# Kernel tuning notes

Hardware: AMD Instinct MI355X
Metric: run time of the kernel (lower is better)

Reference implementation:

```python
import jax, jax.numpy as jnp
import numpy as np

N_KW, N_RT = 100000, 20000
D, H, O = 128, 128, 128
E_A, E_B, E_C = 1600000, 1600000, 320000


def setup_inputs() -> dict:
    key = jax.random.key(0)
    ks = jax.random.split(key, 32)
    inp = {
        "x_kw": jax.random.normal(ks[0], (N_KW, D), jnp.float32),
        "x_rt": jax.random.normal(ks[1], (N_RT, D), jnp.float32),
        "src_a": jax.random.randint(ks[2], (E_A,), 0, N_RT),
        "dst_a": jax.random.randint(ks[3], (E_A,), 0, N_KW),
        "src_b": jax.random.randint(ks[4], (E_B,), 0, N_KW),
        "dst_b": jax.random.randint(ks[5], (E_B,), 0, N_KW),
        "src_c": jax.random.randint(ks[6], (E_C,), 0, N_RT),
        "dst_c": jax.random.randint(ks[7], (E_C,), 0, N_RT),
    }
    # SAGEConv params per relation per layer: W_l (neighbor), b_l, W_r (root, no bias)
    i = 8
    dims = {1: (D, H), 2: (H, O)}
    for layer in (1, 2):
        din, dout = dims[layer]
        for rel in ("a", "b", "c"):
            inp[f"Wl{layer}{rel}"] = jax.random.normal(ks[i], (din, dout), jnp.float32) * 0.05; i += 1
            inp[f"bl{layer}{rel}"] = jnp.zeros((dout,), jnp.float32)
            inp[f"Wr{layer}{rel}"] = jax.random.normal(ks[i], (din, dout), jnp.float32) * 0.05; i += 1
    return inp


def _sage(x_src, x_dst, src, dst, Wl, bl, Wr):
    # PyG SAGEConv (mean aggr): lin_l(mean_j x_src[j]) + lin_r(x_dst)
    n = x_dst.shape[0]
    s = jax.ops.segment_sum(x_src[src], dst, num_segments=n)      # [n, din]
    cnt = jax.ops.segment_sum(jnp.ones_like(dst, dtype=x_src.dtype), dst, num_segments=n)
    mean = s / jnp.maximum(cnt, 1.0)[:, None]
    return mean @ Wl + bl + x_dst @ Wr


def reference(x_kw, x_rt, src_a, dst_a, src_b, dst_b, src_c, dst_c,
              Wl1a, bl1a, Wr1a, Wl1b, bl1b, Wr1b, Wl1c, bl1c, Wr1c,
              Wl2a, bl2a, Wr2a, Wl2b, bl2b, Wr2b, Wl2c, bl2c, Wr2c):
    # layer 1 (HeteroConv aggr='sum' over relations sharing a dst type)
    kw1 = (_sage(x_rt, x_kw, src_a, dst_a, Wl1a, bl1a, Wr1a)
           + _sage(x_kw, x_kw, src_b, dst_b, Wl1b, bl1b, Wr1b))
    rt1 = _sage(x_rt, x_rt, src_c, dst_c, Wl1c, bl1c, Wr1c)
    kw1 = jax.nn.relu(kw1)
    rt1 = jax.nn.relu(rt1)
    # layer 2
    kw2 = (_sage(rt1, kw1, src_a, dst_a, Wl2a, bl2a, Wr2a)
           + _sage(kw1, kw1, src_b, dst_b, Wl2b, bl2b, Wr2b))
    rt2 = _sage(rt1, rt1, src_c, dst_c, Wl2c, bl2c, Wr2c)
    return kw2, rt2
```

## Files before the change

### kernel.cpp

```cpp
#include <hip/hip_runtime.h>

typedef __attribute__((ext_vector_type(8))) short bf16x8;
typedef __attribute__((ext_vector_type(4))) float f32x4;
typedef __attribute__((ext_vector_type(2))) float f32x2;

static __device__ __forceinline__ unsigned short f2bf(float f) {
    unsigned int u = __float_as_uint(f);
    u += 0x7fffu + ((u >> 16) & 1u);
    return (unsigned short)(u >> 16);
}
static __device__ __forceinline__ float bf2f(unsigned short h) {
    return __uint_as_float(((unsigned int)h) << 16);
}

#define BSH 6
#define BUCKET 64
#define NBMAX 1600
#define CHSH 13


struct PrepArgs {
    const float* W[10];
    const float* Wa[10];
    const float* b1a; const float* b1b; const float* b2a; const float* b2b;
};

__global__ void prep_k(PrepArgs pa, unsigned short* __restrict__ Wt,
                       float* __restrict__ bc1, float* __restrict__ bc2) {
    int blk = blockIdx.x;
    if (blk < 640) {
        int slot = blk >> 6;
        int i = ((blk & 63) << 8) + threadIdx.x;
        float v = pa.W[slot][i];
        const float* w2 = pa.Wa[slot];
        if (w2) v += w2[i];
        int k = i >> 7, n = i & 127;
        Wt[slot * 16384 + n * 128 + k] = f2bf(v);
    } else {
        int t = threadIdx.x;
        if (t < 128) bc1[t] = pa.b1a[t] + pa.b1b[t];
        else bc2[t - 128] = pa.b2a[t - 128] + pa.b2b[t - 128];
    }
}


struct Rel {
    const int* src; const int* dst; int E; int nb; int Ndst;
    int hblk0, hnblk;
    int sblk0, snblk;
    int oblk0;
    int* bcnt; int* boff; int* bcur;
    unsigned* pairs; unsigned* ssrc; int* goff; float* invd;
};
struct Rels { Rel r[3]; };

__global__ void bhist3_k(Rels R) {
    const Rel* r;
    int bid = blockIdx.x;
    if (bid < R.r[1].hblk0) r = &R.r[0];
    else if (bid < R.r[2].hblk0) r = &R.r[1];
    else r = &R.r[2];
    __shared__ int h[NBMAX];
    for (int i = threadIdx.x; i < r->nb; i += 256) h[i] = 0;
    __syncthreads();
    for (int e = (bid - r->hblk0) * 256 + threadIdx.x; e < r->E; e += r->hnblk * 256)
        atomicAdd(&h[r->dst[e] >> BSH], 1);
    __syncthreads();
    for (int i = threadIdx.x; i < r->nb; i += 256)
        if (h[i]) atomicAdd(&r->bcnt[i], h[i]);
}

__global__ void bscan3_k(Rels R) {
    const Rel* r = &R.r[blockIdx.x];
    __shared__ int s[1024];
    int t = threadIdx.x;
    int nb = r->nb;
    int e0 = 2 * t, e1 = 2 * t + 1;
    int v0 = (e0 < nb) ? r->bcnt[e0] : 0;
    int v1 = (e1 < nb) ? r->bcnt[e1] : 0;
    s[t] = v0 + v1;
    __syncthreads();
    for (int o = 1; o < 1024; o <<= 1) {
        int x = (t >= o) ? s[t - o] : 0;
        __syncthreads();
        s[t] += x;
        __syncthreads();
    }
    int P = s[t] - (v0 + v1);
    if (e0 <= nb) { r->boff[e0] = P; if (e0 < nb) r->bcur[e0] = 0; }
    if (e1 <= nb) { r->boff[e1] = P + v0; if (e1 < nb) r->bcur[e1] = 0; }
}

__global__ __launch_bounds__(256) void bscatter3_k(Rels R) {
    const Rel* r;
    int bid = blockIdx.x;
    if (bid < R.r[1].sblk0) r = &R.r[0];
    else if (bid < R.r[2].sblk0) r = &R.r[1];
    else r = &R.r[2];
    __shared__ int h[NBMAX];
    __shared__ int base[NBMAX];
    int t = threadIdx.x;
    int nb = r->nb, E = r->E;
    for (int i = t; i < nb; i += 256) h[i] = 0;
    __syncthreads();
    int e0 = (bid - r->sblk0) * 8192;
    for (int i = 0; i < 32; i++) {
        int e = e0 + i * 256 + t;
        if (e < E) atomicAdd(&h[r->dst[e] >> BSH], 1);
    }
    __syncthreads();
    for (int i = t; i < nb; i += 256) {
        int c = h[i];
        base[i] = c ? (r->boff[i] + atomicAdd(&r->bcur[i], c)) : 0;
    }
    __syncthreads();
    for (int i = t; i < nb; i += 256) h[i] = 0;
    __syncthreads();
    for (int i = 0; i < 32; i++) {
        int e = e0 + i * 256 + t;
        if (e < E) {
            int d = r->dst[e];
            int b = d >> BSH;
            int pos = base[b] + atomicAdd(&h[b], 1);
            r->pairs[pos] = ((unsigned)(d & (BUCKET - 1)) << 17) | (unsigned)r->src[e];
        }
    }
}

__global__ __launch_bounds__(256) void sortb3_k(Rels R) {
    const Rel* r;
    int bid = blockIdx.x;
    if (bid < R.r[1].oblk0) r = &R.r[0];
    else if (bid < R.r[2].oblk0) r = &R.r[1];
    else r = &R.r[2];
    int b = bid - r->oblk0;
    __shared__ int cnt[1024];
    __shared__ int sc[256];
    int t = threadIdx.x;
    for (int i = t; i < 1024; i += 256) cnt[i] = 0;
    __syncthreads();
    int j0 = r->boff[b], j1 = r->boff[b + 1];
    for (int j = j0 + t; j < j1; j += 256) {
        unsigned p = r->pairs[j];
        int d = (p >> 17) & 63;
        int ch = (int)((p & 0x1ffffu) >> CHSH); if (ch > 15) ch = 15;
        int bin = ((d & 7) << 7) | ((d >> 3) << 4) | ch;
        atomicAdd(&cnt[bin], 1);
    }
    __syncthreads();
    if (t < 64) {
        int b0 = ((t & 7) << 7) | ((t >> 3) << 4);
        int c = 0;
#pragma unroll
        for (int i = 0; i < 16; i++) c += cnt[b0 + i];
        int dd = (b << BSH) + t;
        if (dd < r->Ndst) r->invd[dd] = 1.f / (float)(c > 0 ? c : 1);
    }
    int c0 = cnt[4 * t], c1 = cnt[4 * t + 1], c2 = cnt[4 * t + 2], c3 = cnt[4 * t + 3];
    int tot = c0 + c1 + c2 + c3;
    sc[t] = tot;
    __syncthreads();
    for (int o = 1; o < 256; o <<= 1) {
        int x = (t >= o) ? sc[t - o] : 0;
        __syncthreads();
        sc[t] += x;
        __syncthreads();
    }
    int base = j0 + sc[t] - tot;
    if ((t & 3) == 0) r->goff[b * 64 + (t >> 2)] = base;
    cnt[4 * t] = base;
    cnt[4 * t + 1] = base + c0;
    cnt[4 * t + 2] = base + c0 + c1;
    cnt[4 * t + 3] = base + c0 + c1 + c2;
    if (t == 0 && b == r->nb - 1) r->goff[r->nb * 64] = r->E;
    __syncthreads();
    for (int j = j0 + t; j < j1; j += 256) {
        unsigned p = r->pairs[j];
        int d = (p >> 17) & 63;
        int ch = (int)((p & 0x1ffffu) >> CHSH); if (ch > 15) ch = 15;
        int bin = ((d & 7) << 7) | ((d >> 3) << 4) | ch;
        int pos = atomicAdd(&cnt[bin], 1);
        r->ssrc[pos] = p & 0x1ffffu;
    }
}


struct GemmJobs {
    const void* Akw; int Nkw;
    const unsigned short* Wk1; const float* bk; unsigned short* Zkw;
    const unsigned short* Wk2; unsigned short* Ckw;
    const void* Art; int Nrt;
    const unsigned short* Wr1; const float* br; unsigned short* Zrt;
    const unsigned short* Wr2; unsigned short* Crt2;
    const unsigned short* Wr3; unsigned short* Crt3;
    int kwBlocks;
};

template <int AF32>
__global__ __launch_bounds__(256) void gemm3_k(GemmJobs G) {
    int bid = blockIdx.x;
    bool iskw = bid < G.kwBlocks;
    const void* A = iskw ? G.Akw : G.Art;
    int N = iskw ? G.Nkw : G.Nrt;
    int lane = threadIdx.x & 63;
    int r16 = lane & 15, g = lane >> 4;
    int row0 = (iskw ? bid : bid - G.kwBlocks) * 64 + (threadIdx.x >> 6) * 16;
    int arow = row0 + r16;
    int arow_c = arow < N ? arow : N - 1;

    bf16x8 af[4];
    if (AF32) {
        const float* Af = (const float*)A + (size_t)arow_c * 128 + g * 8;
#pragma unroll
        for (int kc = 0; kc < 4; kc++) {
            float4 u0 = *(const float4*)(Af + kc * 32);
            float4 u1 = *(const float4*)(Af + kc * 32 + 4);
            bf16x8 r;
            r[0] = (short)f2bf(u0.x); r[1] = (short)f2bf(u0.y);
            r[2] = (short)f2bf(u0.z); r[3] = (short)f2bf(u0.w);
            r[4] = (short)f2bf(u1.x); r[5] = (short)f2bf(u1.y);
            r[6] = (short)f2bf(u1.z); r[7] = (short)f2bf(u1.w);
            af[kc] = r;
        }
    } else {
        const bf16x8* Ar = (const bf16x8*)((const unsigned short*)A + (size_t)arow_c * 128);
#pragma unroll
        for (int kc = 0; kc < 4; kc++) af[kc] = Ar[kc * 4 + g];
    }

    if (iskw) {
        f32x4 acc1[8], acc2[8];
#pragma unroll
        for (int ct = 0; ct < 8; ct++) { f32x4 z = {0.f,0.f,0.f,0.f}; acc1[ct] = z; acc2[ct] = z; }
#pragma unroll
        for (int kc = 0; kc < 4; kc++) {
#pragma unroll
            for (int ct = 0; ct < 8; ct++) {
                int wo = ((ct * 16 + r16) << 7) + kc * 32 + g * 8;
                bf16x8 b1 = *(const bf16x8*)(G.Wk1 + wo);
                acc1[ct] = __builtin_amdgcn_mfma_f32_16x16x32_bf16(af[kc], b1, acc1[ct], 0, 0, 0);
                bf16x8 b2 = *(const bf16x8*)(G.Wk2 + wo);
                acc2[ct] = __builtin_amdgcn_mfma_f32_16x16x32_bf16(af[kc], b2, acc2[ct], 0, 0, 0);
            }
        }
#pragma unroll
        for (int ct = 0; ct < 8; ct++) {
            int col = ct * 16 + r16;
            float bb = G.bk[col];
#pragma unroll
            for (int j = 0; j < 4; j++) {
                int r = row0 + g * 4 + j;
                if (r < N) {
                    G.Zkw[(size_t)r * 128 + col] = f2bf(acc1[ct][j] + bb);
                    G.Ckw[(size_t)r * 128 + col] = f2bf(acc2[ct][j]);
                }
            }
        }
    } else {
        f32x4 acc1[8], acc2[8], acc3[8];
#pragma unroll
        for (int ct = 0; ct < 8; ct++) {
            f32x4 z = {0.f,0.f,0.f,0.f}; acc1[ct] = z; acc2[ct] = z; acc3[ct] = z;
        }
#pragma unroll
        for (int kc = 0; kc < 4; kc++) {
#pragma unroll
            for (int ct = 0; ct < 8; ct++) {
                int wo = ((ct * 16 + r16) << 7) + kc * 32 + g * 8;
                bf16x8 b1 = *(const bf16x8*)(G.Wr1 + wo);
                acc1[ct] = __builtin_amdgcn_mfma_f32_16x16x32_bf16(af[kc], b1, acc1[ct], 0, 0, 0);
                bf16x8 b2 = *(const bf16x8*)(G.Wr2 + wo);
                acc2[ct] = __builtin_amdgcn_mfma_f32_16x16x32_bf16(af[kc], b2, acc2[ct], 0, 0, 0);
                bf16x8 b3 = *(const bf16x8*)(G.Wr3 + wo);
                acc3[ct] = __builtin_amdgcn_mfma_f32_16x16x32_bf16(af[kc], b3, acc3[ct], 0, 0, 0);
            }
        }
#pragma unroll
        for (int ct = 0; ct < 8; ct++) {
            int col = ct * 16 + r16;
            float bb = G.br[col];
#pragma unroll
            for (int j = 0; j < 4; j++) {
                int r = row0 + g * 4 + j;
                if (r < N) {
                    G.Zrt[(size_t)r * 128 + col] = f2bf(acc1[ct][j] + bb);
                    G.Crt2[(size_t)r * 128 + col] = f2bf(acc2[ct][j]);
                    G.Crt3[(size_t)r * 128 + col] = f2bf(acc3[ct][j]);
                }
            }
        }
    }
}

struct AggJob {
    const unsigned short* Zin; int Ndst;
    const unsigned* sp0; const int* goff0; const float* invd0; const unsigned short* Y0;
    const unsigned* sp1; const int* goff1; const float* invd1; const unsigned short* Y1;
    int nrel;
    float* OutF; unsigned short* OutB;
};

template <int RELU, int OUTBF16>
__global__ __launch_bounds__(512) void bagg2_k(AggJob JK, AggJob JR, int kwBlocks) {
    __shared__ float acc[BUCKET * 128];
    bool iskw = blockIdx.x < kwBlocks;
    AggJob J = iskw ? JK : JR;
    int b = iskw ? blockIdx.x : blockIdx.x - kwBlocks;
    int t = threadIdx.x;
    int dst0 = b << BSH;
    int nrow = J.Ndst - dst0; if (nrow > BUCKET) nrow = BUCKET;

    for (int c = t; c < BUCKET * 32; c += 512) {
        int r = c >> 5, m = c & 31;
        float z0 = 0.f, z1 = 0.f, z2 = 0.f, z3 = 0.f;
        if (r < nrow) {
            ushort4 z = *(const ushort4*)(J.Zin + (size_t)(dst0 + r) * 128 + (m << 2));
            z0 = bf2f(z.x); z1 = bf2f(z.y); z2 = bf2f(z.z); z3 = bf2f(z.w);
        }
        acc[r * 128 + m] = z0;
        acc[r * 128 + 32 + m] = z1;
        acc[r * 128 + 64 + m] = z2;
        acc[r * 128 + 96 + m] = z3;
    }
    __syncthreads();

    int w = t >> 6, lane = t & 63;
    int h = lane >> 5, q = lane & 31;
#pragma unroll 1
    for (int rel = 0; rel < J.nrel; rel++) {
        const unsigned* sp = rel ? J.sp1 : J.sp0;
        const int* goff = rel ? J.goff1 : J.goff0;
        const float* invd = rel ? J.invd1 : J.invd0;
        const unsigned short* Y = rel ? J.Y1 : J.Y0;
#pragma unroll 1
        for (int r = 0; r < 8; r++) {
            int g = b * 64 + w * 8 + r;
            int jg0 = goff[g], jg1 = goff[g + 1];
            if (jg0 >= jg1) continue;
            int d = (r << 3) | w;
            f32x2 a01 = {0.f, 0.f}, a23 = {0.f, 0.f};
#pragma unroll 1
            for (int j = jg0; j < jg1; j += 16) {
                uint2 v[8];
#pragma unroll
                for (int k = 0; k < 8; k++) {
                    int e = j + 2 * k + h;
                    e = e < jg1 ? e : jg1 - 1;
                    int s = (int)sp[e];
                    v[k] = *(const uint2*)(Y + ((size_t)s << 7) + (q << 2));
                }
#pragma unroll
                for (int k = 0; k < 8; k++) {
                    bool ok = (j + 2 * k + h) < jg1;
                    unsigned vx = ok ? v[k].x : 0u;
                    unsigned vy = ok ? v[k].y : 0u;
                    f32x2 x01 = { __uint_as_float(vx << 16),
                                  __uint_as_float(vx & 0xffff0000u) };
                    f32x2 x23 = { __uint_as_float(vy << 16),
                                  __uint_as_float(vy & 0xffff0000u) };
                    a01 += x01;
                    a23 += x23;
                }
            }
            a01.x += __shfl_xor(a01.x, 32); a01.y += __shfl_xor(a01.y, 32);
            a23.x += __shfl_xor(a23.x, 32); a23.y += __shfl_xor(a23.y, 32);
            float inv = invd[dst0 + d];
            float v0 = (h ? a23.x : a01.x) * inv;
            float v1 = (h ? a23.y : a01.y) * inv;
            int ba = d * 128 + q + h * 64;
            acc[ba] += v0;
            acc[ba + 32] += v1;
        }
    }
    __syncthreads();
    for (int c = t; c < BUCKET * 32; c += 512) {
        int r = c >> 5, m = c & 31;
        if (r < nrow) {
            float x0 = acc[r * 128 + m];
            float x1 = acc[r * 128 + 32 + m];
            float x2 = acc[r * 128 + 64 + m];
            float x3 = acc[r * 128 + 96 + m];
            if (RELU) {
                x0 = fmaxf(x0, 0.f); x1 = fmaxf(x1, 0.f);
                x2 = fmaxf(x2, 0.f); x3 = fmaxf(x3, 0.f);
            }
            size_t o = (size_t)(dst0 + r) * 128 + (m << 2);
            if (OUTBF16) {
                ushort4 ov;
                ov.x = f2bf(x0); ov.y = f2bf(x1); ov.z = f2bf(x2); ov.w = f2bf(x3);
                *(ushort4*)(J.OutB + o) = ov;
            } else {
                *(float4*)(J.OutF + o) = make_float4(x0, x1, x2, x3);
            }
        }
    }
}


static inline size_t align256(size_t x) { return (x + 255) & ~size_t(255); }

extern "C" void kernel_launch(void* const* d_in, const int* in_sizes, int n_in,
                              void* d_out, int out_size, void* d_ws, size_t ws_size,
                              hipStream_t stream) {
    const float* x_kw = (const float*)d_in[0];
    const float* x_rt = (const float*)d_in[1];
    const int* src_a = (const int*)d_in[2];
    const int* dst_a = (const int*)d_in[3];
    const int* src_b = (const int*)d_in[4];
    const int* dst_b = (const int*)d_in[5];
    const int* src_c = (const int*)d_in[6];
    const int* dst_c = (const int*)d_in[7];
    const float *Wl1a = (const float*)d_in[8],  *bl1a = (const float*)d_in[9],  *Wr1a = (const float*)d_in[10];
    const float *Wl1b = (const float*)d_in[11], *bl1b = (const float*)d_in[12], *Wr1b = (const float*)d_in[13];
    const float *Wl1c = (const float*)d_in[14], *bl1c = (const float*)d_in[15], *Wr1c = (const float*)d_in[16];
    const float *Wl2a = (const float*)d_in[17], *bl2a = (const float*)d_in[18], *Wr2a = (const float*)d_in[19];
    const float *Wl2b = (const float*)d_in[20], *bl2b = (const float*)d_in[21], *Wr2b = (const float*)d_in[22];
    const float *Wl2c = (const float*)d_in[23], *bl2c = (const float*)d_in[24], *Wr2c = (const float*)d_in[25];

    const int NKW = in_sizes[0] / 128;
    const int NRT = in_sizes[1] / 128;
    const int EA = in_sizes[2], EB = in_sizes[4], EC = in_sizes[6];
    const int nb_kw = (NKW + BUCKET - 1) / BUCKET;
    const int nb_rt = (NRT + BUCKET - 1) / BUCKET;

    char* ws = (char*)d_ws;
    size_t off = 0;
    auto alloc = [&](size_t bytes) -> char* {
        off = align256(off);
        char* p = ws + off;
        off += bytes;
        return p;
    };
    unsigned short* Wt = (unsigned short*)alloc(10 * 16384 * 2);
    float* bc1 = (float*)alloc(128 * 4);
    float* bc2 = (float*)alloc(128 * 4);
    int* bcnt3 = (int*)alloc(3 * NBMAX * 4);
    int* bcur3 = (int*)alloc(3 * NBMAX * 4);
    int* boff_a = (int*)alloc((NBMAX + 1) * 4);
    int* boff_b = (int*)alloc((NBMAX + 1) * 4);
    int* boff_c = (int*)alloc((NBMAX + 1) * 4);
    int* goff_a = (int*)alloc(((size_t)nb_kw * 64 + 1) * 4);
    int* goff_b = (int*)alloc(((size_t)nb_kw * 64 + 1) * 4);
    int* goff_c = (int*)alloc(((size_t)nb_rt * 64 + 1) * 4);
    float* invd_a = (float*)alloc((size_t)NKW * 4);
    float* invd_b = (float*)alloc((size_t)NKW * 4);
    float* invd_c = (float*)alloc((size_t)NRT * 4);
    unsigned* pairs_a = (unsigned*)alloc((size_t)EA * 4);
    unsigned* pairs_b = (unsigned*)alloc((size_t)EB * 4);
    unsigned* pairs_c = (unsigned*)alloc((size_t)EC * 4);
    unsigned* sp_a = (unsigned*)alloc((size_t)EA * 4);
    unsigned* sp_b = (unsigned*)alloc((size_t)EB * 4);
    unsigned* sp_c = (unsigned*)alloc((size_t)EC * 4);
    unsigned short* Yb = (unsigned short*)alloc((size_t)NKW * 128 * 2);
    unsigned short* Zkw = (unsigned short*)alloc((size_t)NKW * 128 * 2);
    unsigned short* Zrt = (unsigned short*)alloc((size_t)NRT * 128 * 2);
    unsigned short* kw1_bf = (unsigned short*)alloc((size_t)NKW * 128 * 2);
    unsigned short* rt1_bf = (unsigned short*)alloc((size_t)NRT * 128 * 2);
    (void)ws_size;
    unsigned short* Ya = (unsigned short*)pairs_b;
    unsigned short* Yc = (unsigned short*)pairs_a;

    float* out_kw = (float*)d_out;
    float* out_rt = out_kw + (size_t)NKW * 128;

    PrepArgs pa;
    pa.W[0] = Wr1a; pa.Wa[0] = Wr1b;
    pa.W[1] = Wl1a; pa.Wa[1] = nullptr;
    pa.W[2] = Wl1b; pa.Wa[2] = nullptr;
    pa.W[3] = Wl1c; pa.Wa[3] = nullptr;
    pa.W[4] = Wr1c; pa.Wa[4] = nullptr;
    pa.W[5] = Wr2a; pa.Wa[5] = Wr2b;
    pa.W[6] = Wl2a; pa.Wa[6] = nullptr;
    pa.W[7] = Wl2b; pa.Wa[7] = nullptr;
    pa.W[8] = Wl2c; pa.Wa[8] = nullptr;
    pa.W[9] = Wr2c; pa.Wa[9] = nullptr;
    pa.b1a = bl1a; pa.b1b = bl1b; pa.b2a = bl2a; pa.b2b = bl2b;
    prep_k<<<641, 256, 0, stream>>>(pa, Wt, bc1, bc2);
    unsigned short* W0 = Wt + 0 * 16384;
    unsigned short* W1 = Wt + 1 * 16384;
    unsigned short* W2 = Wt + 2 * 16384;
    unsigned short* W3 = Wt + 3 * 16384;
    unsigned short* W4 = Wt + 4 * 16384;
    unsigned short* W5 = Wt + 5 * 16384;
    unsigned short* W6 = Wt + 6 * 16384;
    unsigned short* W7 = Wt + 7 * 16384;
    unsigned short* W8 = Wt + 8 * 16384;
    unsigned short* W9 = Wt + 9 * 16384;

    hipMemsetAsync(bcnt3, 0, 3 * NBMAX * 4, stream);
    Rels R;
    int hA = 128, hB = 128, hC = 64;
    int sA = (EA + 8191) / 8192, sB = (EB + 8191) / 8192, sC = (EC + 8191) / 8192;
    R.r[0] = {src_a, dst_a, EA, nb_kw, NKW, 0, hA, 0, sA, 0,
              bcnt3, boff_a, bcur3, pairs_a, sp_a, goff_a, invd_a};
    R.r[1] = {src_b, dst_b, EB, nb_kw, NKW, hA, hB, sA, sB, nb_kw,
              bcnt3 + NBMAX, boff_b, bcur3 + NBMAX, pairs_b, sp_b, goff_b, invd_b};
    R.r[2] = {src_c, dst_c, EC, nb_rt, NRT, hA + hB, hC, sA + sB, sC, 2 * nb_kw,
              bcnt3 + 2 * NBMAX, boff_c, bcur3 + 2 * NBMAX, pairs_c, sp_c, goff_c, invd_c};
    bhist3_k<<<hA + hB + hC, 256, 0, stream>>>(R);
    bscan3_k<<<3, 1024, 0, stream>>>(R);
    bscatter3_k<<<sA + sB + sC, 256, 0, stream>>>(R);
    sortb3_k<<<2 * nb_kw + nb_rt, 256, 0, stream>>>(R);

    const int kwB = (NKW + 63) / 64, rtB = (NRT + 63) / 64;

    GemmJobs G1;
    G1.Akw = x_kw; G1.Nkw = NKW; G1.Wk1 = W0; G1.bk = bc1; G1.Zkw = Zkw; G1.Wk2 = W2; G1.Ckw = Yb;
    G1.Art = x_rt; G1.Nrt = NRT; G1.Wr1 = W4; G1.br = bl1c; G1.Zrt = Zrt;
    G1.Wr2 = W1; G1.Crt2 = Ya; G1.Wr3 = W3; G1.Crt3 = Yc;
    G1.kwBlocks = kwB;
    gemm3_k<1><<<kwB + rtB, 256, 0, stream>>>(G1);

    AggJob JK1 = {Zkw, NKW, sp_a, goff_a, invd_a, Ya, sp_b, goff_b, invd_b, Yb, 2,
                  nullptr, kw1_bf};
    AggJob JR1 = {Zrt, NRT, sp_c, goff_c, invd_c, Yc, nullptr, nullptr, nullptr, nullptr, 1,
                  nullptr, rt1_bf};
    bagg2_k<1, 1><<<nb_kw + nb_rt, 512, 0, stream>>>(JK1, JR1, nb_kw);

    GemmJobs G2;
    G2.Akw = kw1_bf; G2.Nkw = NKW; G2.Wk1 = W5; G2.bk = bc2; G2.Zkw = Zkw; G2.Wk2 = W7; G2.Ckw = Yb;
    G2.Art = rt1_bf; G2.Nrt = NRT; G2.Wr1 = W9; G2.br = bl2c; G2.Zrt = Zrt;
    G2.Wr2 = W6; G2.Crt2 = Ya; G2.Wr3 = W8; G2.Crt3 = Yc;
    G2.kwBlocks = kwB;
    gemm3_k<0><<<kwB + rtB, 256, 0, stream>>>(G2);

    AggJob JK2 = {Zkw, NKW, sp_a, goff_a, invd_a, Ya, sp_b, goff_b, invd_b, Yb, 2,
                  out_kw, nullptr};
    AggJob JR2 = {Zrt, NRT, sp_c, goff_c, invd_c, Yc, nullptr, nullptr, nullptr, nullptr, 1,
                  out_rt, nullptr};
    bagg2_k<0, 0><<<nb_kw + nb_rt, 512, 0, stream>>>(JK2, JR2, nb_kw);
}
```

Before: 580.3 us.

## Fuse layer-2 projection GEMMs into layer-1 aggregation epilogue

The layer-1 aggregation kernel now applies ReLU in shared memory and runs the layer-2 MFMA projections (root plus bias, and neighbor transforms) directly on its 64-row tile. The separate layer-2 GEMM launch and the bf16 round trip of the kw1/rt1 hidden features through global memory go away. The shared accumulator rows are padded to a stride of 130 floats to avoid LDS bank conflicts, and buffers are reassigned so later aggregation reads do not race with epilogue writes. In exchange, the aggregation kernel carries more registers under a tighter launch bound, and the rt blocks serialize two matrices on half the waves.

```diff
diff --git a/kernel.cpp b/kernel.cpp
--- a/kernel.cpp
+++ b/kernel.cpp
@@ -17,6 +17,7 @@
 #define BUCKET 64
 #define NBMAX 1600
 #define CHSH 13
+#define ASTRIDE 130
 
 
 struct PrepArgs {
@@ -186,21 +187,20 @@
 
 
 struct GemmJobs {
-    const void* Akw; int Nkw;
+    const float* Akw; int Nkw;
     const unsigned short* Wk1; const float* bk; unsigned short* Zkw;
     const unsigned short* Wk2; unsigned short* Ckw;
-    const void* Art; int Nrt;
+    const float* Art; int Nrt;
     const unsigned short* Wr1; const float* br; unsigned short* Zrt;
     const unsigned short* Wr2; unsigned short* Crt2;
     const unsigned short* Wr3; unsigned short* Crt3;
     int kwBlocks;
 };
 
-template <int AF32>
 __global__ __launch_bounds__(256) void gemm3_k(GemmJobs G) {
     int bid = blockIdx.x;
     bool iskw = bid < G.kwBlocks;
-    const void* A = iskw ? G.Akw : G.Art;
+    const float* A = iskw ? G.Akw : G.Art;
     int N = iskw ? G.Nkw : G.Nrt;
     int lane = threadIdx.x & 63;
     int r16 = lane & 15, g = lane >> 4;
@@ -209,23 +209,19 @@
     int arow_c = arow < N ? arow : N - 1;
 
     bf16x8 af[4];
-    if (AF32) {
-        const float* Af = (const float*)A + (size_t)arow_c * 128 + g * 8;
+    {
+        const float* Af = A + (size_t)arow_c * 128 + g * 8;
 #pragma unroll
         for (int kc = 0; kc < 4; kc++) {
             float4 u0 = *(const float4*)(Af + kc * 32);
             float4 u1 = *(const float4*)(Af + kc * 32 + 4);
-            bf16x8 r;
-            r[0] = (short)f2bf(u0.x); r[1] = (short)f2bf(u0.y);
-            r[2] = (short)f2bf(u0.z); r[3] = (short)f2bf(u0.w);
-            r[4] = (short)f2bf(u1.x); r[5] = (short)f2bf(u1.y);
-            r[6] = (short)f2bf(u1.z); r[7] = (short)f2bf(u1.w);
-            af[kc] = r;
-        }
-    } else {
-        const bf16x8* Ar = (const bf16x8*)((const unsigned short*)A + (size_t)arow_c * 128);
-#pragma unroll
-        for (int kc = 0; kc < 4; kc++) af[kc] = Ar[kc * 4 + g];
+            bf16x8 rr;
+            rr[0] = (short)f2bf(u0.x); rr[1] = (short)f2bf(u0.y);
+            rr[2] = (short)f2bf(u0.z); rr[3] = (short)f2bf(u0.w);
+            rr[4] = (short)f2bf(u1.x); rr[5] = (short)f2bf(u1.y);
+            rr[6] = (short)f2bf(u1.z); rr[7] = (short)f2bf(u1.w);
+            af[kc] = rr;
+        }
     }
 
     if (iskw) {
@@ -292,18 +288,22 @@
     }
 }
 
+
 struct AggJob {
     const unsigned short* Zin; int Ndst;
     const unsigned* sp0; const int* goff0; const float* invd0; const unsigned short* Y0;
     const unsigned* sp1; const int* goff1; const float* invd1; const unsigned short* Y1;
     int nrel;
     float* OutF; unsigned short* OutB;
+    const unsigned short* Wg1; const float* bg1; unsigned short* Cg1;
+    const unsigned short* Wg2; unsigned short* Cg2;
+    const unsigned short* Wg3; unsigned short* Cg3;
 };
 
-template <int RELU, int OUTBF16>
-__global__ __launch_bounds__(512) void bagg2_k(AggJob JK, AggJob JR, int kwBlocks) {
-    __shared__ float acc[BUCKET * 128];
-    bool iskw = blockIdx.x < kwBlocks;
+template <int RELU, int OUTBF16, int GEPI>
+__global__ __launch_bounds__(512, 8) void bagg2_k(AggJob JK, AggJob JR, int kwBlocks) {
+    __shared__ float acc[BUCKET * ASTRIDE];
+    bool iskw = blockIdx.x < (unsigned)kwBlocks;
     AggJob J = iskw ? JK : JR;
     int b = iskw ? blockIdx.x : blockIdx.x - kwBlocks;
     int t = threadIdx.x;
@@ -317,10 +317,10 @@
             ushort4 z = *(const ushort4*)(J.Zin + (size_t)(dst0 + r) * 128 + (m << 2));
             z0 = bf2f(z.x); z1 = bf2f(z.y); z2 = bf2f(z.z); z3 = bf2f(z.w);
         }
-        acc[r * 128 + m] = z0;
-        acc[r * 128 + 32 + m] = z1;
-        acc[r * 128 + 64 + m] = z2;
-        acc[r * 128 + 96 + m] = z3;
+        acc[r * ASTRIDE + m] = z0;
+        acc[r * ASTRIDE + 32 + m] = z1;
+        acc[r * ASTRIDE + 64 + m] = z2;
+        acc[r * ASTRIDE + 96 + m] = z3;
     }
     __syncthreads();
 
@@ -362,24 +362,84 @@
                     a23 += x23;
                 }
             }
-            a01.x += __shfl_xor(a01.x, 32); a01.y += __shfl_xor(a01.y, 32);
-            a23.x += __shfl_xor(a23.x, 32); a23.y += __shfl_xor(a23.y, 32);
+            a01[0] += __shfl_xor(a01[0], 32); a01[1] += __shfl_xor(a01[1], 32);
+            a23[0] += __shfl_xor(a23[0], 32); a23[1] += __shfl_xor(a23[1], 32);
             float inv = invd[dst0 + d];
-            float v0 = (h ? a23.x : a01.x) * inv;
-            float v1 = (h ? a23.y : a01.y) * inv;
-            int ba = d * 128 + q + h * 64;
+            float v0 = (h ? a23[0] : a01[0]) * inv;
+            float v1 = (h ? a23[1] : a01[1]) * inv;
+            int ba = d * ASTRIDE + q + h * 64;
             acc[ba] += v0;
             acc[ba + 32] += v1;
         }
     }
     __syncthreads();
+
+    if (GEPI) {
+        for (int c = t; c < BUCKET * 32; c += 512) {
+            int r = c >> 5, m = c & 31;
+            int ba = r * ASTRIDE + m;
+            acc[ba] = fmaxf(acc[ba], 0.f);
+            acc[ba + 32] = fmaxf(acc[ba + 32], 0.f);
+            acc[ba + 64] = fmaxf(acc[ba + 64], 0.f);
+            acc[ba + 96] = fmaxf(acc[ba + 96], 0.f);
+        }
+        __syncthreads();
+        int r16 = lane & 15, gg = lane >> 4;
+        int rg = (w & 3) * 16;
+        bf16x8 af[4];
+        int rbase = (rg + r16) * ASTRIDE;
+#pragma unroll
+        for (int kc = 0; kc < 4; kc++) {
+            int m2 = 2 * (kc * 4 + gg);
+            float2 p0 = *(const float2*)&acc[rbase + m2];
+            float2 p1 = *(const float2*)&acc[rbase + 32 + m2];
+            float2 p2 = *(const float2*)&acc[rbase + 64 + m2];
+            float2 p3 = *(const float2*)&acc[rbase + 96 + m2];
+            bf16x8 rr;
+            rr[0] = (short)f2bf(p0.x); rr[1] = (short)f2bf(p1.x);
+            rr[2] = (short)f2bf(p2.x); rr[3] = (short)f2bf(p3.x);
+            rr[4] = (short)f2bf(p0.y); rr[5] = (short)f2bf(p1.y);
+            rr[6] = (short)f2bf(p2.y); rr[7] = (short)f2bf(p3.y);
+            af[kc] = rr;
+        }
+        const unsigned short* WtA; unsigned short* CA; const float* biasA;
+        const unsigned short* WtB = nullptr; unsigned short* CB = nullptr;
+        if ((w >> 2) == 0) { WtA = J.Wg1; CA = J.Cg1; biasA = J.bg1; }
+        else {
+            WtA = J.Wg2; CA = J.Cg2; biasA = nullptr;
+            if (J.Wg3) { WtB = J.Wg3; CB = J.Cg3; }
+        }
+        auto run_mat = [&](const unsigned short* Wt_, unsigned short* C_, const float* bias) {
+#pragma unroll 1
+            for (int ct = 0; ct < 8; ct++) {
+                f32x4 a4 = {0.f, 0.f, 0.f, 0.f};
+#pragma unroll
+                for (int kc = 0; kc < 4; kc++) {
+                    bf16x8 bfrag = *(const bf16x8*)(Wt_ + ((ct * 16 + r16) << 7) + kc * 32 + gg * 8);
+                    a4 = __builtin_amdgcn_mfma_f32_16x16x32_bf16(af[kc], bfrag, a4, 0, 0, 0);
+                }
+                int col = ct * 16 + r16;
+                float bb = bias ? bias[col] : 0.f;
+#pragma unroll
+                for (int jj = 0; jj < 4; jj++) {
+                    int rloc = rg + gg * 4 + jj;
+                    if (rloc < nrow)
+                        C_[(size_t)(dst0 + rloc) * 128 + col] = f2bf(a4[jj] + bb);
+                }
+            }
+        };
+        run_mat(WtA, CA, biasA);
+        if (WtB) run_mat(WtB, CB, nullptr);
+        return;
+    }
+
     for (int c = t; c < BUCKET * 32; c += 512) {
         int r = c >> 5, m = c & 31;
         if (r < nrow) {
-            float x0 = acc[r * 128 + m];
-            float x1 = acc[r * 128 + 32 + m];
-            float x2 = acc[r * 128 + 64 + m];
-            float x3 = acc[r * 128 + 96 + m];
+            float x0 = acc[r * ASTRIDE + m];
+            float x1 = acc[r * ASTRIDE + 32 + m];
+            float x2 = acc[r * ASTRIDE + 64 + m];
+            float x3 = acc[r * ASTRIDE + 96 + m];
             if (RELU) {
                 x0 = fmaxf(x0, 0.f); x1 = fmaxf(x1, 0.f);
                 x2 = fmaxf(x2, 0.f); x3 = fmaxf(x3, 0.f);
@@ -451,14 +511,15 @@
     unsigned* sp_a = (unsigned*)alloc((size_t)EA * 4);
     unsigned* sp_b = (unsigned*)alloc((size_t)EB * 4);
     unsigned* sp_c = (unsigned*)alloc((size_t)EC * 4);
+    unsigned short* Ya = (unsigned short*)alloc((size_t)NRT * 128 * 2);
     unsigned short* Yb = (unsigned short*)alloc((size_t)NKW * 128 * 2);
+    unsigned short* Yc = (unsigned short*)alloc((size_t)NRT * 128 * 2);
     unsigned short* Zkw = (unsigned short*)alloc((size_t)NKW * 128 * 2);
     unsigned short* Zrt = (unsigned short*)alloc((size_t)NRT * 128 * 2);
-    unsigned short* kw1_bf = (unsigned short*)alloc((size_t)NKW * 128 * 2);
-    unsigned short* rt1_bf = (unsigned short*)alloc((size_t)NRT * 128 * 2);
+    unsigned short* Yb2 = (unsigned short*)alloc((size_t)NKW * 128 * 2);
     (void)ws_size;
-    unsigned short* Ya = (unsigned short*)pairs_b;
-    unsigned short* Yc = (unsigned short*)pairs_a;
+    unsigned short* Ya2 = (unsigned short*)pairs_a;
+    unsigned short* Yc2 = (unsigned short*)pairs_b;
 
     float* out_kw = (float*)d_out;
     float* out_rt = out_kw + (size_t)NKW * 128;
@@ -509,24 +570,25 @@
     G1.Art = x_rt; G1.Nrt = NRT; G1.Wr1 = W4; G1.br = bl1c; G1.Zrt = Zrt;
     G1.Wr2 = W1; G1.Crt2 = Ya; G1.Wr3 = W3; G1.Crt3 = Yc;
     G1.kwBlocks = kwB;
-    gemm3_k<1><<<kwB + rtB, 256, 0, stream>>>(G1);
+    gemm3_k<<<kwB + rtB, 256, 0, stream>>>(G1);
 
     AggJob JK1 = {Zkw, NKW, sp_a, goff_a, invd_a, Ya, sp_b, goff_b, invd_b, Yb, 2,
-                  nullptr, kw1_bf};
+                  nullptr, nullptr,
+                  W5, bc2, Zkw,
+                  W7, Yb2,
+                  nullptr, nullptr};
     AggJob JR1 = {Zrt, NRT, sp_c, goff_c, invd_c, Yc, nullptr, nullptr, nullptr, nullptr, 1,
-                  nullptr, rt1_bf};
-    bagg2_k<1, 1><<<nb_kw + nb_rt, 512, 0, stream>>>(JK1, JR1, nb_kw);
-
-    GemmJobs G2;
-    G2.Akw = kw1_bf; G2.Nkw = NKW; G2.Wk1 = W5; G2.bk = bc2; G2.Zkw = Zkw; G2.Wk2 = W7; G2.Ckw = Yb;
-    G2.Art = rt1_bf; G2.Nrt = NRT; G2.Wr1 = W9; G2.br = bl2c; G2.Zrt = Zrt;
-    G2.Wr2 = W6; G2.Crt2 = Ya; G2.Wr3 = W8; G2.Crt3 = Yc;
-    G2.kwBlocks = kwB;
-    gemm3_k<0><<<kwB + rtB, 256, 0, stream>>>(G2);
-
-    AggJob JK2 = {Zkw, NKW, sp_a, goff_a, invd_a, Ya, sp_b, goff_b, invd_b, Yb, 2,
-                  out_kw, nullptr};
-    AggJob JR2 = {Zrt, NRT, sp_c, goff_c, invd_c, Yc, nullptr, nullptr, nullptr, nullptr, 1,
-                  out_rt, nullptr};
-    bagg2_k<0, 0><<<nb_kw + nb_rt, 512, 0, stream>>>(JK2, JR2, nb_kw);
-}
+                  nullptr, nullptr,
+                  W9, bl2c, Zrt,
+                  W6, Ya2,
+                  W8, Yc2};
+    bagg2_k<1, 1, 1><<<nb_kw + nb_rt, 512, 0, stream>>>(JK1, JR1, nb_kw);
+
+    AggJob JK2 = {Zkw, NKW, sp_a, goff_a, invd_a, Ya2, sp_b, goff_b, invd_b, Yb2, 2,
+                  out_kw, nullptr,
+                  nullptr, nullptr, nullptr, nullptr, nullptr, nullptr, nullptr};
+    AggJob JR2 = {Zrt, NRT, sp_c, goff_c, invd_c, Yc2, nullptr, nullptr, nullptr, nullptr, 1,
+                  out_rt, nullptr,
+                  nullptr, nullptr, nullptr, nullptr, nullptr, nullptr, nullptr};
+    bagg2_k<0, 0, 0><<<nb_kw + nb_rt, 512, 0, stream>>>(JK2, JR2, nb_kw);
+}
```

After: 554.9 us. -4.4%, faster.
